# Optimization experiments

Measured on AMD Instinct MI355X. Metric: run time of the kernel, lower is better.

## Reference

```python
import jax, jax.numpy as jnp
import numpy as np

B, T, D, E, C = 4, 4096, 2048, 8, 1024
H = D // E  # per-expert hidden = out_features // num_experts = 256


def setup_inputs() -> dict:
    key = jax.random.key(0)
    ks = jax.random.split(key, 7)
    x = jax.random.normal(ks[0], (B, T, D), dtype=jnp.float32)
    # nn.Linear-style init scale ~ 1/sqrt(fan_in)
    W1 = jax.random.normal(ks[1], (E, H, D), dtype=jnp.float32) / np.sqrt(D)
    b1 = jax.random.normal(ks[2], (E, H), dtype=jnp.float32) / np.sqrt(D)
    W2 = jax.random.normal(ks[3], (E, D, H), dtype=jnp.float32) / np.sqrt(D)
    b2 = jax.random.normal(ks[4], (D,), dtype=jnp.float32) / np.sqrt(D)
    expert_indices = jax.random.randint(ks[5], (B, E, C), 0, T, dtype=jnp.int32)
    expert_gate = jax.random.uniform(ks[6], (B, E, C), dtype=jnp.float32)
    return {"x": x, "W1": W1, "b1": b1, "W2": W2, "b2": b2,
            "expert_indices": expert_indices, "expert_gate": expert_gate,
            "num_tokens": T}


def reference(x, W1, b1, W2, b2, expert_indices, expert_gate, num_tokens):
    # x: (B,T,D); expert_indices/expert_gate: (B,E,C)
    Bb = x.shape[0]
    Ee, Cc = expert_indices.shape[1], expert_indices.shape[2]
    b_idx = jnp.arange(Bb)[:, None, None]
    # dispatch: gather tokens per expert -> (B,E,C,D)
    sel = x[b_idx, expert_indices]
    # contract: per-expert GEMM -> (B,E,C,H)
    h = jnp.einsum('becd,ehd->bech', sel, W1) + b1[None, :, None, :]
    h = jax.nn.gelu(h, approximate=False)
    # expand: per-expert GEMM -> (B,E,C,D), shared output bias
    y = jnp.einsum('bech,eoh->beco', h, W2) + b2
    y = y * expert_gate[..., None]
    # combine: gated scatter-add back to token positions -> (B,T,D)
    out = jnp.zeros((Bb, num_tokens, x.shape[2]), dtype=x.dtype)
    out = out.at[jnp.arange(Bb)[:, None], expert_indices.reshape(Bb, Ee * Cc)].add(
        y.reshape(Bb, Ee * Cc, -1))
    return out
```

## Files before the change

kernel.cpp:

```cpp
#include <hip/hip_runtime.h>
#include <hip/hip_bf16.h>
#include <math.h>

#define B_ 4
#define T_ 4096
#define D_ 2048
#define E_ 8
#define C_ 1024
#define H_ 256
#define SLOTCAP 32

typedef unsigned short u16;
typedef unsigned long long u64;
typedef __attribute__((ext_vector_type(8))) short short8;
typedef __attribute__((ext_vector_type(4))) float f32x4;

__device__ __forceinline__ u16 f2bf_n(float f) {
    union { __hip_bfloat16 b; u16 u; } v;
    v.b = __float2bfloat16(f);
    return v.u;
}
__device__ __forceinline__ float bf2f(u16 u) {
    union { unsigned u; float f; } v; v.u = ((unsigned)u) << 16;
    return v.f;
}

__device__ __forceinline__ int swz(int row, int chunk) {
    return (row << 6) + ((chunk ^ (row & 7)) << 3);
}

__device__ __forceinline__ void gload16(const void* g, void* l) {
    __builtin_amdgcn_global_load_lds(
        (const __attribute__((address_space(1))) void*)g,
        (__attribute__((address_space(3))) void*)l, 16, 0, 0);
}

__global__ __launch_bounds__(256) void conv_w1_img(
    const float* __restrict__ W1, u16* __restrict__ img)
{
    const int cid = blockIdx.x * 256 + threadIdx.x;
    const int e = cid >> 16;
    const int kt = (cid >> 11) & 31;
    const int row = (cid >> 3) & 255;
    const int sc = cid & 7;
    const float* s = W1 + (((size_t)e * 256 + row) * 2048 + kt * 64
                           + ((sc ^ (row & 7)) << 3));
    f32x4 v0 = *reinterpret_cast<const f32x4*>(s);
    f32x4 v1 = *reinterpret_cast<const f32x4*>(s + 4);
    u16 o[8];
    #pragma unroll
    for (int j = 0; j < 4; ++j) { o[j] = f2bf_n(v0[j]); o[j + 4] = f2bf_n(v1[j]); }
    *reinterpret_cast<short8*>(img + (size_t)cid * 8) =
        *reinterpret_cast<const short8*>(o);
}

__global__ __launch_bounds__(256) void conv_w2_img(
    const float* __restrict__ W2, u16* __restrict__ img)
{
    const int cid = blockIdx.x * 256 + threadIdx.x;
    const int e = cid >> 16;
    const int nt = (cid >> 13) & 7;
    const int kt = (cid >> 11) & 3;
    const int row = (cid >> 3) & 255;
    const int sc = cid & 7;
    const float* s = W2 + (((size_t)e * 2048 + nt * 256 + row) * 256 + kt * 64
                           + ((sc ^ (row & 7)) << 3));
    f32x4 v0 = *reinterpret_cast<const f32x4*>(s);
    f32x4 v1 = *reinterpret_cast<const f32x4*>(s + 4);
    u16 o[8];
    #pragma unroll
    for (int j = 0; j < 4; ++j) { o[j] = f2bf_n(v0[j]); o[j + 4] = f2bf_n(v1[j]); }
    *reinterpret_cast<short8*>(img + (size_t)cid * 8) =
        *reinterpret_cast<const short8*>(o);
}

__global__ __launch_bounds__(256) void zero_cnt(int* __restrict__ cnt)
{
    const int i = (blockIdx.x * 256 + threadIdx.x) * 4;
    *reinterpret_cast<f32x4*>(cnt + i) = (f32x4){0.f, 0.f, 0.f, 0.f};
}

__global__ __launch_bounds__(256, 2) void gemm1_v11(
    const float* __restrict__ x, const u16* __restrict__ W1img,
    const float* __restrict__ b1, const int* __restrict__ idx,
    u16* __restrict__ Himg)
{
    const int be = blockIdx.x;
    const int mt = blockIdx.y;
    const int b = be >> 3, e = be & 7;
    const int m0 = mt * 64;

    __shared__ __align__(16) u16 As[2][4096];
    __shared__ __align__(16) u16 Bs[2][16384];

    const int tid = threadIdx.x;
    const int lane = tid & 63, wid = tid >> 6;
    const int l15 = lane & 15, lk = lane >> 4;

    const int row8 = tid >> 2, sc2 = (tid & 3) * 2;
    const int tok = idx[(b * E_ + e) * C_ + m0 + row8];
    const float* aRow = x + ((size_t)b * T_ + tok) * D_ + sc2 * 8;
    const int aOff0 = swz(row8, sc2), aOff1 = swz(row8, sc2 + 1);

    const u16* bSrcLane = W1img + (size_t)e * 32 * 16384 + wid * 512 + lane * 8;
    const int bofs = wid * 512;

    f32x4 pa[4];

#define A_LOAD(t)                                                             \
    do {                                                                      \
        pa[0] = *reinterpret_cast<const f32x4*>(aRow + (t) * 64);             \
        pa[1] = *reinterpret_cast<const f32x4*>(aRow + (t) * 64 + 4);         \
        pa[2] = *reinterpret_cast<const f32x4*>(aRow + (t) * 64 + 8);         \
        pa[3] = *reinterpret_cast<const f32x4*>(aRow + (t) * 64 + 12);        \
    } while (0)

#define A_WRITE(buf)                                                          \
    do {                                                                      \
        short8 s0, s1;                                                        \
        _Pragma("unroll")                                                     \
        for (int r = 0; r < 4; ++r) {                                         \
            s0[r] = (short)f2bf_n(pa[0][r]); s0[r + 4] = (short)f2bf_n(pa[1][r]); \
            s1[r] = (short)f2bf_n(pa[2][r]); s1[r + 4] = (short)f2bf_n(pa[3][r]); \
        }                                                                     \
        *reinterpret_cast<short8*>(&As[buf][aOff0]) = s0;                     \
        *reinterpret_cast<short8*>(&As[buf][aOff1]) = s1;                     \
    } while (0)

#define B_ISSUE(buf, t)                                                       \
    do {                                                                      \
        const u16* b_ = bSrcLane + (size_t)(t) * 16384;                       \
        _Pragma("unroll")                                                     \
        for (int j = 0; j < 8; ++j)                                           \
            gload16(b_ + j * 2048, &Bs[buf][j * 2048 + bofs]);                \
    } while (0)

    f32x4 acc[4][4];
    #pragma unroll
    for (int i = 0; i < 4; ++i)
        #pragma unroll
        for (int j = 0; j < 4; ++j)
            acc[i][j] = (f32x4){0.f, 0.f, 0.f, 0.f};

    A_LOAD(0); A_WRITE(0);
    A_LOAD(1); A_WRITE(1);
    B_ISSUE(0, 0);
    B_ISSUE(1, 1);
    A_LOAD(2);
    asm volatile("s_waitcnt lgkmcnt(0)" ::: "memory");

    const int NT = D_ / 64;
    for (int t = 0; t < NT; ++t) {
        const int cur = t & 1;
        if (t < NT - 1) asm volatile("s_waitcnt vmcnt(12)" ::: "memory");
        else            asm volatile("s_waitcnt vmcnt(0)" ::: "memory");
        __builtin_amdgcn_s_barrier();
        __builtin_amdgcn_sched_barrier(0);
        #pragma unroll
        for (int kk = 0; kk < 2; ++kk) {
            short8 af[4], bfr[4];
            #pragma unroll
            for (int m = 0; m < 4; ++m) {
                const int row = m * 16 + l15;
                af[m] = *reinterpret_cast<const short8*>(
                    &As[cur][swz(row, kk * 4 + lk)]);
            }
            #pragma unroll
            for (int n = 0; n < 4; ++n) {
                const int row = wid * 64 + n * 16 + l15;
                bfr[n] = *reinterpret_cast<const short8*>(
                    &Bs[cur][swz(row, kk * 4 + lk)]);
            }
            __builtin_amdgcn_s_setprio(1);
            #pragma unroll
            for (int m = 0; m < 4; ++m)
                #pragma unroll
                for (int n = 0; n < 4; ++n)
                    acc[m][n] = __builtin_amdgcn_mfma_f32_16x16x32_bf16(
                        bfr[n], af[m], acc[m][n], 0, 0, 0);
            __builtin_amdgcn_s_setprio(0);
        }
        asm volatile("s_waitcnt lgkmcnt(0)" ::: "memory");
        __builtin_amdgcn_s_barrier();
        __builtin_amdgcn_sched_barrier(0);
        if (t + 2 < NT) A_WRITE(cur);
        if (t + 3 < NT) A_LOAD(t + 3);
        if (t + 2 < NT) B_ISSUE(cur, t + 2);
    }
#undef A_LOAD
#undef A_WRITE
#undef B_ISSUE

    const size_t hblk = ((size_t)(be * 16 + mt) * 4 + wid) * 4096;
    #pragma unroll
    for (int m = 0; m < 4; ++m) {
        const int row = m * 16 + l15;
        #pragma unroll
        for (int n = 0; n < 4; ++n) {
            const int hb = wid * 64 + n * 16 + lk * 4;
            f32x4 bias = *reinterpret_cast<const f32x4*>(&b1[e * H_ + hb]);
            u16 o[4];
            #pragma unroll
            for (int r = 0; r < 4; ++r) {
                float h = acc[m][n][r] + bias[r];
                float g = 0.5f * h * (1.0f + erff(h * 0.70710678118f));
                o[r] = f2bf_n(g);
            }
            const int lc = (n * 2 + (lk >> 1)) ^ (row & 7);
            u16* p = Himg + hblk + row * 64 + lc * 8 + (lk & 1) * 4;
            *reinterpret_cast<u64*>(p) = *reinterpret_cast<const u64*>(o);
        }
    }
}

__global__ __launch_bounds__(512) void gemm2_v8(
    const u16* __restrict__ Himg, const u16* __restrict__ W2img,
    const float* __restrict__ b2, const float* __restrict__ gate,
    u16* __restrict__ Ybuf)
{
    const int be = blockIdx.x;
    const int nt = blockIdx.y;
    const int b = be >> 3, e = be & 7;
    const int n0 = nt * 256;

    __shared__ __align__(16) u16 As[16384];
    __shared__ __align__(16) u16 Bs[65536];

    const int tid = threadIdx.x;
    const int lane = tid & 63, wid = tid >> 6;
    const int wm = wid >> 2, wn = wid & 3;
    const int l15 = lane & 15, lk = lane >> 4;
    const int wofs = wid * 512;

    const u16* bPanel = W2img + (size_t)(e * 8 + nt) * 65536;
    #pragma unroll
    for (int j = 0; j < 16; ++j)
        gload16(bPanel + (size_t)(j * 512 + tid) * 8, &Bs[j * 4096 + wofs]);

    const u16* aBase = Himg + (size_t)(be * 16) * 16384 + (size_t)tid * 8;

#define A_ISSUE(mt)                                                           \
    do {                                                                      \
        const u16* a_ = aBase + (size_t)(mt) * 16384;                         \
        gload16(a_,          &As[wofs]);                                      \
        gload16(a_ + 4096,   &As[4096 + wofs]);                               \
        gload16(a_ + 8192,   &As[8192 + wofs]);                               \
        gload16(a_ + 12288,  &As[12288 + wofs]);                              \
    } while (0)

    A_ISSUE(0);

    f32x4 bias[4];
    #pragma unroll
    for (int n = 0; n < 4; ++n)
        bias[n] = *reinterpret_cast<const f32x4*>(
            &b2[n0 + wn * 64 + n * 16 + lk * 4]);

    const int gbase = (b * E_ + e) * C_ + wm * 32 + l15;
    const size_t ybase = (size_t)(b * E_ + e) * C_;

    float gc0 = gate[gbase];
    float gc1 = gate[gbase + 16];

    asm volatile("s_waitcnt vmcnt(0)" ::: "memory");
    __builtin_amdgcn_s_barrier();
    __builtin_amdgcn_sched_barrier(0);

    for (int mt = 0; mt < 16; ++mt) {
        f32x4 acc[2][4];
        #pragma unroll
        for (int i = 0; i < 2; ++i)
            #pragma unroll
            for (int j = 0; j < 4; ++j)
                acc[i][j] = (f32x4){0.f, 0.f, 0.f, 0.f};

        #pragma unroll
        for (int t = 0; t < 4; ++t) {
            #pragma unroll
            for (int kk = 0; kk < 2; ++kk) {
                short8 af[2], bfr[4];
                #pragma unroll
                for (int m = 0; m < 2; ++m) {
                    const int row = wm * 32 + m * 16 + l15;
                    af[m] = *reinterpret_cast<const short8*>(
                        &As[t * 4096 + swz(row, kk * 4 + lk)]);
                }
                #pragma unroll
                for (int n = 0; n < 4; ++n) {
                    const int row = wn * 64 + n * 16 + l15;
                    bfr[n] = *reinterpret_cast<const short8*>(
                        &Bs[t * 16384 + swz(row, kk * 4 + lk)]);
                }
                __builtin_amdgcn_s_setprio(1);
                #pragma unroll
                for (int m = 0; m < 2; ++m)
                    #pragma unroll
                    for (int n = 0; n < 4; ++n)
                        acc[m][n] = __builtin_amdgcn_mfma_f32_16x16x32_bf16(
                            bfr[n], af[m], acc[m][n], 0, 0, 0);
                __builtin_amdgcn_s_setprio(0);
            }
        }

        asm volatile("s_waitcnt lgkmcnt(0)" ::: "memory");
        __builtin_amdgcn_s_barrier();
        __builtin_amdgcn_sched_barrier(0);

        if (mt < 15) A_ISSUE(mt + 1);
        float gn0 = 0.f, gn1 = 0.f;
        if (mt < 15) {
            gn0 = gate[gbase + (mt + 1) * 64];
            gn1 = gate[gbase + (mt + 1) * 64 + 16];
        }

        #pragma unroll
        for (int m = 0; m < 2; ++m) {
            const int cl = wm * 32 + m * 16 + l15;
            const float g = (m == 0) ? gc0 : gc1;
            u16* rowp = Ybuf + (ybase + mt * 64 + cl) * (size_t)D_ + n0;
            #pragma unroll
            for (int n = 0; n < 4; ++n) {
                const int db = wn * 64 + n * 16 + lk * 4;
                u16 o[4];
                #pragma unroll
                for (int r = 0; r < 4; ++r)
                    o[r] = f2bf_n((acc[m][n][r] + bias[n][r]) * g);
                *reinterpret_cast<u64*>(rowp + db) =
                    *reinterpret_cast<const u64*>(o);
            }
        }

        if (mt < 15) {
            asm volatile("s_waitcnt vmcnt(18)" ::: "memory");
            __builtin_amdgcn_s_barrier();
            __builtin_amdgcn_sched_barrier(0);
        }
        gc0 = gn0; gc1 = gn1;
    }
#undef A_ISSUE
}

__global__ __launch_bounds__(256) void fill_kernel(
    const int* __restrict__ idx, int* __restrict__ cnt,
    int* __restrict__ slots)
{
    int i = blockIdx.x * 256 + threadIdx.x;
    if (i >= B_ * E_ * C_) return;
    int b = i / (E_ * C_);
    int slot = i % (E_ * C_);
    int t = idx[i];
    int p = atomicAdd(&cnt[b * T_ + t], 1);
    if (p < SLOTCAP) slots[(b * T_ + t) * SLOTCAP + p] = slot;
}

__global__ __launch_bounds__(256) void combine_kernel(
    const u16* __restrict__ Ybuf, const int* __restrict__ cnt,
    const int* __restrict__ slots, float* __restrict__ out)
{
    const int bt = blockIdx.x;
    const int tid = threadIdx.x;
    __shared__ int sl[SLOTCAP];
    int n = cnt[bt];
    n = n > SLOTCAP ? SLOTCAP : n;
    if (tid < n) sl[tid] = slots[bt * SLOTCAP + tid];
    __syncthreads();
    const int b = bt >> 12;
    float a[8] = {0.f, 0.f, 0.f, 0.f, 0.f, 0.f, 0.f, 0.f};
    for (int s = 0; s < n; ++s) {
        const u16* yrow = Ybuf + ((size_t)b * (E_ * C_) + sl[s]) * D_ + tid * 8;
        short8 v = *reinterpret_cast<const short8*>(yrow);
        #pragma unroll
        for (int j = 0; j < 8; ++j) a[j] += bf2f((u16)v[j]);
    }
    float* orow = out + (size_t)bt * D_ + tid * 8;
    *reinterpret_cast<f32x4*>(orow)     = (f32x4){a[0], a[1], a[2], a[3]};
    *reinterpret_cast<f32x4*>(orow + 4) = (f32x4){a[4], a[5], a[6], a[7]};
}

extern "C" void kernel_launch(void* const* d_in, const int* in_sizes, int n_in,
                              void* d_out, int out_size, void* d_ws, size_t ws_size,
                              hipStream_t stream) {
    const float* x    = (const float*)d_in[0];
    const float* W1   = (const float*)d_in[1];
    const float* b1   = (const float*)d_in[2];
    const float* W2   = (const float*)d_in[3];
    const float* b2   = (const float*)d_in[4];
    const int*   idx  = (const int*)d_in[5];
    const float* gate = (const float*)d_in[6];
    float* out = (float*)d_out;

    const size_t nW = (size_t)E_ * H_ * D_;
    const size_t nH = (size_t)B_ * E_ * C_ * H_;
    const size_t nY = (size_t)B_ * E_ * C_ * D_;

    u16* W1img = (u16*)d_ws;
    u16* W2img = W1img + nW;
    u16* Himg  = W2img + nW;
    u16* Ybuf  = Himg + nH;
    int* cnt   = (int*)(Ybuf + nY);
    int* slots = cnt + (size_t)B_ * T_;

    zero_cnt<<<(B_ * T_) / 1024, 256, 0, stream>>>(cnt);
    conv_w1_img<<<2048, 256, 0, stream>>>(W1, W1img);
    conv_w2_img<<<2048, 256, 0, stream>>>(W2, W2img);
    fill_kernel<<<(B_ * E_ * C_) / 256, 256, 0, stream>>>(idx, cnt, slots);

    gemm1_v11<<<dim3(32, 16), 256, 0, stream>>>(x, W1img, b1, idx, Himg);
    gemm2_v8<<<dim3(32, 8), 512, 0, stream>>>(Himg, W2img, b2, gate, Ybuf);
    combine_kernel<<<B_ * T_, 256, 0, stream>>>(Ybuf, cnt, slots, out);
}
```

Measured before the change: 219.0 us.

## Enlarge GEMM1 tile to 128x256 with 512 threads and register-staged W1 loads

```diff
diff --git a/kernel.cpp b/kernel.cpp
--- a/kernel.cpp
+++ b/kernel.cpp
@@ -35,23 +35,15 @@
         (__attribute__((address_space(3))) void*)l, 16, 0, 0);
 }
 
-__global__ __launch_bounds__(256) void conv_w1_img(
-    const float* __restrict__ W1, u16* __restrict__ img)
-{
-    const int cid = blockIdx.x * 256 + threadIdx.x;
-    const int e = cid >> 16;
-    const int kt = (cid >> 11) & 31;
-    const int row = (cid >> 3) & 255;
-    const int sc = cid & 7;
-    const float* s = W1 + (((size_t)e * 256 + row) * 2048 + kt * 64
-                           + ((sc ^ (row & 7)) << 3));
-    f32x4 v0 = *reinterpret_cast<const f32x4*>(s);
-    f32x4 v1 = *reinterpret_cast<const f32x4*>(s + 4);
-    u16 o[8];
-    #pragma unroll
-    for (int j = 0; j < 4; ++j) { o[j] = f2bf_n(v0[j]); o[j + 4] = f2bf_n(v1[j]); }
-    *reinterpret_cast<short8*>(img + (size_t)cid * 8) =
-        *reinterpret_cast<const short8*>(o);
+__global__ __launch_bounds__(256) void conv_f32_bf16(
+    const float* __restrict__ src, u16* __restrict__ dst, int n)
+{
+    int i = (blockIdx.x * 256 + threadIdx.x) * 4;
+    if (i >= n) return;
+    f32x4 v = *reinterpret_cast<const f32x4*>(src + i);
+    u16 o[4];
+    o[0] = f2bf_n(v[0]); o[1] = f2bf_n(v[1]); o[2] = f2bf_n(v[2]); o[3] = f2bf_n(v[3]);
+    *reinterpret_cast<u64*>(dst + i) = *reinterpret_cast<const u64*>(o);
 }
 
 __global__ __launch_bounds__(256) void conv_w2_img(
@@ -80,42 +72,63 @@
     *reinterpret_cast<f32x4*>(cnt + i) = (f32x4){0.f, 0.f, 0.f, 0.f};
 }
 
-__global__ __launch_bounds__(256, 2) void gemm1_v11(
-    const float* __restrict__ x, const u16* __restrict__ W1img,
+__global__ __launch_bounds__(512) void gemm1_v12(
+    const float* __restrict__ x, const u16* __restrict__ W1bf,
     const float* __restrict__ b1, const int* __restrict__ idx,
     u16* __restrict__ Himg)
 {
     const int be = blockIdx.x;
-    const int mt = blockIdx.y;
+    const int mt2 = blockIdx.y;
     const int b = be >> 3, e = be & 7;
-    const int m0 = mt * 64;
-
-    __shared__ __align__(16) u16 As[2][4096];
-    __shared__ __align__(16) u16 Bs[2][16384];
+    const int m0 = mt2 * 128;
+
+    __shared__ __align__(16) u16 As[2][128 * 64];
+    __shared__ __align__(16) u16 Bs[2][256 * 64];
+    __shared__ int toks[128];
+    __shared__ float bs1[256];
 
     const int tid = threadIdx.x;
+    if (tid < 128) toks[tid] = idx[(b * E_ + e) * C_ + m0 + tid];
+    if (tid < 256) bs1[tid] = b1[e * H_ + tid];
+    __syncthreads();
+
     const int lane = tid & 63, wid = tid >> 6;
+    const int wm = wid >> 2, wn = wid & 3;
     const int l15 = lane & 15, lk = lane >> 4;
 
-    const int row8 = tid >> 2, sc2 = (tid & 3) * 2;
-    const int tok = idx[(b * E_ + e) * C_ + m0 + row8];
-    const float* aRow = x + ((size_t)b * T_ + tok) * D_ + sc2 * 8;
-    const int aOff0 = swz(row8, sc2), aOff1 = swz(row8, sc2 + 1);
-
-    const u16* bSrcLane = W1img + (size_t)e * 32 * 16384 + wid * 512 + lane * 8;
-    const int bofs = wid * 512;
+    const int ar = tid >> 2, ac0 = tid & 3;
+    const float* aRow = x + (size_t)b * (T_ * (size_t)D_)
+                          + (size_t)toks[ar] * D_;
+    const int br = tid >> 1, bc0 = (tid & 1) * 4;
+    const u16* bRow = W1bf + ((size_t)e * H_ + br) * D_;
+
+    const int aOff0 = swz(ar, ac0), aOff1 = swz(ar, ac0 + 4);
+    int bOff[4];
+    #pragma unroll
+    for (int j = 0; j < 4; ++j) bOff[j] = swz(br, bc0 + j);
+
+    f32x4 acc[4][4];
+    #pragma unroll
+    for (int i = 0; i < 4; ++i)
+        #pragma unroll
+        for (int j = 0; j < 4; ++j)
+            acc[i][j] = (f32x4){0.f, 0.f, 0.f, 0.f};
 
     f32x4 pa[4];
-
-#define A_LOAD(t)                                                             \
+    short8 pb[4];
+
+#define G1_LOAD(k)                                                            \
     do {                                                                      \
-        pa[0] = *reinterpret_cast<const f32x4*>(aRow + (t) * 64);             \
-        pa[1] = *reinterpret_cast<const f32x4*>(aRow + (t) * 64 + 4);         \
-        pa[2] = *reinterpret_cast<const f32x4*>(aRow + (t) * 64 + 8);         \
-        pa[3] = *reinterpret_cast<const f32x4*>(aRow + (t) * 64 + 12);        \
+        pa[0] = *reinterpret_cast<const f32x4*>(aRow + (k) + ac0 * 8);        \
+        pa[1] = *reinterpret_cast<const f32x4*>(aRow + (k) + ac0 * 8 + 4);    \
+        pa[2] = *reinterpret_cast<const f32x4*>(aRow + (k) + (ac0 + 4) * 8);  \
+        pa[3] = *reinterpret_cast<const f32x4*>(aRow + (k) + (ac0 + 4) * 8 + 4);\
+        _Pragma("unroll")                                                     \
+        for (int j = 0; j < 4; ++j)                                           \
+            pb[j] = *reinterpret_cast<const short8*>(bRow + (k) + (bc0 + j) * 8);\
     } while (0)
 
-#define A_WRITE(buf)                                                          \
+#define G1_WRITE(buf)                                                         \
     do {                                                                      \
         short8 s0, s1;                                                        \
         _Pragma("unroll")                                                     \
@@ -125,49 +138,34 @@
         }                                                                     \
         *reinterpret_cast<short8*>(&As[buf][aOff0]) = s0;                     \
         *reinterpret_cast<short8*>(&As[buf][aOff1]) = s1;                     \
+        _Pragma("unroll")                                                     \
+        for (int j = 0; j < 4; ++j)                                           \
+            *reinterpret_cast<short8*>(&Bs[buf][bOff[j]]) = pb[j];            \
     } while (0)
 
-#define B_ISSUE(buf, t)                                                       \
-    do {                                                                      \
-        const u16* b_ = bSrcLane + (size_t)(t) * 16384;                       \
-        _Pragma("unroll")                                                     \
-        for (int j = 0; j < 8; ++j)                                           \
-            gload16(b_ + j * 2048, &Bs[buf][j * 2048 + bofs]);                \
-    } while (0)
-
-    f32x4 acc[4][4];
-    #pragma unroll
-    for (int i = 0; i < 4; ++i)
-        #pragma unroll
-        for (int j = 0; j < 4; ++j)
-            acc[i][j] = (f32x4){0.f, 0.f, 0.f, 0.f};
-
-    A_LOAD(0); A_WRITE(0);
-    A_LOAD(1); A_WRITE(1);
-    B_ISSUE(0, 0);
-    B_ISSUE(1, 1);
-    A_LOAD(2);
+    G1_LOAD(0);
+    G1_WRITE(0);
+    G1_LOAD(64);
     asm volatile("s_waitcnt lgkmcnt(0)" ::: "memory");
+    __builtin_amdgcn_s_barrier();
 
     const int NT = D_ / 64;
     for (int t = 0; t < NT; ++t) {
         const int cur = t & 1;
-        if (t < NT - 1) asm volatile("s_waitcnt vmcnt(12)" ::: "memory");
-        else            asm volatile("s_waitcnt vmcnt(0)" ::: "memory");
-        __builtin_amdgcn_s_barrier();
-        __builtin_amdgcn_sched_barrier(0);
+        if (t + 1 < NT) G1_WRITE(cur ^ 1);
+        if (t + 2 < NT) G1_LOAD((t + 2) * 64);
         #pragma unroll
         for (int kk = 0; kk < 2; ++kk) {
             short8 af[4], bfr[4];
             #pragma unroll
             for (int m = 0; m < 4; ++m) {
-                const int row = m * 16 + l15;
+                const int row = wm * 64 + m * 16 + l15;
                 af[m] = *reinterpret_cast<const short8*>(
                     &As[cur][swz(row, kk * 4 + lk)]);
             }
             #pragma unroll
             for (int n = 0; n < 4; ++n) {
-                const int row = wid * 64 + n * 16 + l15;
+                const int row = wn * 64 + n * 16 + l15;
                 bfr[n] = *reinterpret_cast<const short8*>(
                     &Bs[cur][swz(row, kk * 4 + lk)]);
             }
@@ -182,27 +180,23 @@
         }
         asm volatile("s_waitcnt lgkmcnt(0)" ::: "memory");
         __builtin_amdgcn_s_barrier();
-        __builtin_amdgcn_sched_barrier(0);
-        if (t + 2 < NT) A_WRITE(cur);
-        if (t + 3 < NT) A_LOAD(t + 3);
-        if (t + 2 < NT) B_ISSUE(cur, t + 2);
     }
-#undef A_LOAD
-#undef A_WRITE
-#undef B_ISSUE
-
-    const size_t hblk = ((size_t)(be * 16 + mt) * 4 + wid) * 4096;
+#undef G1_LOAD
+#undef G1_WRITE
+
     #pragma unroll
     for (int m = 0; m < 4; ++m) {
-        const int row = m * 16 + l15;
+        const int cl = wm * 64 + m * 16 + l15;
+        const int row = cl & 63;
+        const size_t hblk =
+            ((size_t)(be * 16 + mt2 * 2 + (cl >> 6)) * 4 + wn) * 4096;
         #pragma unroll
         for (int n = 0; n < 4; ++n) {
-            const int hb = wid * 64 + n * 16 + lk * 4;
-            f32x4 bias = *reinterpret_cast<const f32x4*>(&b1[e * H_ + hb]);
+            const int hb = wn * 64 + n * 16 + lk * 4;
             u16 o[4];
             #pragma unroll
             for (int r = 0; r < 4; ++r) {
-                float h = acc[m][n][r] + bias[r];
+                float h = acc[m][n][r] + bs1[hb + r];
                 float g = 0.5f * h * (1.0f + erff(h * 0.70710678118f));
                 o[r] = f2bf_n(g);
             }
@@ -393,19 +387,19 @@
     const size_t nH = (size_t)B_ * E_ * C_ * H_;
     const size_t nY = (size_t)B_ * E_ * C_ * D_;
 
-    u16* W1img = (u16*)d_ws;
-    u16* W2img = W1img + nW;
+    u16* W1bf  = (u16*)d_ws;
+    u16* W2img = W1bf + nW;
     u16* Himg  = W2img + nW;
     u16* Ybuf  = Himg + nH;
     int* cnt   = (int*)(Ybuf + nY);
     int* slots = cnt + (size_t)B_ * T_;
 
     zero_cnt<<<(B_ * T_) / 1024, 256, 0, stream>>>(cnt);
-    conv_w1_img<<<2048, 256, 0, stream>>>(W1, W1img);
+    conv_f32_bf16<<<(int)(nW / 1024), 256, 0, stream>>>(W1, W1bf, (int)nW);
     conv_w2_img<<<2048, 256, 0, stream>>>(W2, W2img);
     fill_kernel<<<(B_ * E_ * C_) / 256, 256, 0, stream>>>(idx, cnt, slots);
 
-    gemm1_v11<<<dim3(32, 16), 256, 0, stream>>>(x, W1img, b1, idx, Himg);
+    gemm1_v12<<<dim3(32, 8), 512, 0, stream>>>(x, W1bf, b1, idx, Himg);
     gemm2_v8<<<dim3(32, 8), 512, 0, stream>>>(Himg, W2img, b2, gate, Ybuf);
     combine_kernel<<<B_ * T_, 256, 0, stream>>>(Ybuf, cnt, slots, out);
 }
```

Result: faster. 203.1 us (median of 2 runs) (-7.3%).
